# Kernel tuning notes

Measured on AMD Instinct MI355X. Metric: run time of the kernel, lower is better.

## Reference

```python
import jax, jax.numpy as jnp
import numpy as np

HIDDEN = 1024
HEADS = 16
HEAD_DIM = HIDDEN // HEADS
EPS = 1e-5


def setup_inputs() -> dict:
    key = jax.random.key(0)
    ks = jax.random.split(key, 9)
    B, S, H = 2, 2048, HIDDEN
    scale = 1.0 / np.sqrt(H)
    inp = {
        "hidden_states": jax.random.normal(ks[0], (B, S, H), dtype=jnp.float32),
        "Wq": jax.random.normal(ks[1], (H, H), dtype=jnp.float32) * scale,
        "bq": jnp.zeros((H,), jnp.float32),
        "Wk": jax.random.normal(ks[2], (H, H), dtype=jnp.float32) * scale,
        "bk": jnp.zeros((H,), jnp.float32),
        "Wv": jax.random.normal(ks[3], (H, H), dtype=jnp.float32) * scale,
        "bv": jnp.zeros((H,), jnp.float32),
        "Wo": jax.random.normal(ks[4], (H, H), dtype=jnp.float32) * scale,
        "bo": jnp.zeros((H,), jnp.float32),
        "gamma": jnp.ones((H,), jnp.float32),
        "beta": jnp.zeros((H,), jnp.float32),
    }
    return inp


def reference(hidden_states, Wq, bq, Wk, bk, Wv, bv, Wo, bo, gamma, beta):
    B, S, H = hidden_states.shape
    residual = hidden_states

    def shape(x):  # [B,S,H] -> [B,heads,S,head_dim]
        return x.reshape(B, S, HEADS, HEAD_DIM).transpose(0, 2, 1, 3)

    q = shape(hidden_states @ Wq + bq)
    k = shape(hidden_states @ Wk + bk)
    v = shape(hidden_states @ Wv + bv)

    scores = jnp.einsum("bhqd,bhkd->bhqk", q, k) / jnp.sqrt(
        jnp.asarray(HEAD_DIM, hidden_states.dtype))
    probs = jax.nn.softmax(scores, axis=-1)
    context = jnp.einsum("bhqk,bhkd->bhqd", probs, v)
    context = context.transpose(0, 2, 1, 3).reshape(B, S, H)

    output = context @ Wo + bo
    x = output + residual
    mu = jnp.mean(x, axis=-1, keepdims=True)
    var = jnp.mean(jnp.square(x - mu), axis=-1, keepdims=True)
    return (x - mu) * jax.lax.rsqrt(var + EPS) * gamma + beta
```

## Files before the change

### kernel.cpp

```cpp
#include <hip/hip_runtime.h>
#include <hip/hip_bf16.h>
#include <math.h>

#define HIDDEN 1024
#define HEADS 16
#define HEAD_DIM 64
#define EPS 1e-5f

typedef __attribute__((ext_vector_type(8))) short bf16x8;
typedef __attribute__((ext_vector_type(4))) float f32x4;

#if defined(__has_builtin)
#if __has_builtin(__builtin_amdgcn_exp2f)
#define EXP2(x) __builtin_amdgcn_exp2f(x)
#endif
#endif
#ifndef EXP2
#define EXP2(x) exp2f(x)
#endif

#define QSCALE 0.18033688011112042f

__device__ __forceinline__ short f2bf(float f) {
    union { float f; unsigned u; } v; v.f = f;
    unsigned r = v.u + 0x7fffu + ((v.u >> 16) & 1u);
    return (short)(r >> 16);
}

__global__ __launch_bounds__(256) void cast_bf16_kernel(
    const float* __restrict__ in, short* __restrict__ out, int n)
{
    int i = (blockIdx.x * 256 + threadIdx.x) * 4;
    if (i >= n) return;
    float4 v = *(const float4*)(in + i);
    short o[4] = { f2bf(v.x), f2bf(v.y), f2bf(v.z), f2bf(v.w) };
    *(uint2*)(out + i) = *(uint2*)o;
}

__global__ __launch_bounds__(256) void transpose_cast_kernel(
    const float* __restrict__ W, short* __restrict__ Wt, int Kd, int Nd,
    float scale)
{
    __shared__ short tile[32][33];
    int n0 = blockIdx.x * 32;
    int k0 = blockIdx.y * 32;
    int tx = threadIdx.x & 31;
    int ty = threadIdx.x >> 5;
    #pragma unroll
    for (int i = 0; i < 32; i += 8)
        tile[ty + i][tx] = f2bf(W[(size_t)(k0 + ty + i) * Nd + n0 + tx] * scale);
    __syncthreads();
    #pragma unroll
    for (int i = 0; i < 32; i += 8)
        Wt[(size_t)(n0 + ty + i) * Kd + k0 + tx] = tile[tx][ty + i];
}

__global__ __launch_bounds__(256) void concat_bias_kernel(
    const float* __restrict__ bq, const float* __restrict__ bk,
    const float* __restrict__ bv, float* __restrict__ b3)
{
    int i = blockIdx.x * 256 + threadIdx.x;
    if (i >= 3072) return;
    float v = (i < 1024) ? bq[i] * QSCALE
            : (i < 2048) ? bk[i - 1024] : bv[i - 2048];
    b3[i] = v;
}

__global__ __launch_bounds__(256) void gemm_bt_mfma(
    const short* __restrict__ A, const short* __restrict__ Bt,
    const float* __restrict__ bias,
    void* __restrict__ C0, int ldc0,
    void* __restrict__ C1, int split_col, int ldc1,
    int M, int N, int K, int out_bf16)
{
    __shared__ short As[128][40];
    __shared__ short Bs[128][40];
    const int tid = threadIdx.x;
    const int wave = tid >> 6, lane = tid & 63;
    const int ln16 = lane & 15, quad = lane >> 4;
    const int wm = (wave >> 1) * 64, wn = (wave & 1) * 64;
    const int brow = blockIdx.y * 128, bcol = blockIdx.x * 128;

    f32x4 acc[4][4];
    #pragma unroll
    for (int mt = 0; mt < 4; ++mt)
        #pragma unroll
        for (int nt = 0; nt < 4; ++nt) acc[mt][nt] = (f32x4){0.f, 0.f, 0.f, 0.f};

    for (int k0 = 0; k0 < K; k0 += 32) {
        #pragma unroll
        for (int i = 0; i < 2; ++i) {
            int idx = tid + i * 256;
            int r = idx >> 2;
            int c0 = (idx & 3) * 8;
            *(uint4*)&As[r][c0] = *(const uint4*)(A + (size_t)(brow + r) * K + k0 + c0);
            *(uint4*)&Bs[r][c0] = *(const uint4*)(Bt + (size_t)(bcol + r) * K + k0 + c0);
        }
        __syncthreads();
        bf16x8 af[4], bf[4];
        #pragma unroll
        for (int mt = 0; mt < 4; ++mt)
            af[mt] = *(const bf16x8*)&As[wm + mt * 16 + ln16][quad * 8];
        #pragma unroll
        for (int nt = 0; nt < 4; ++nt)
            bf[nt] = *(const bf16x8*)&Bs[wn + nt * 16 + ln16][quad * 8];
        #pragma unroll
        for (int mt = 0; mt < 4; ++mt)
            #pragma unroll
            for (int nt = 0; nt < 4; ++nt)
                acc[mt][nt] = __builtin_amdgcn_mfma_f32_16x16x32_bf16(
                    af[mt], bf[nt], acc[mt][nt], 0, 0, 0);
        __syncthreads();
    }

    void* Cp = C0; int ld = ldc0; int coff = 0;
    if (bcol >= split_col) { Cp = C1; ld = ldc1; coff = split_col; }

    #pragma unroll
    for (int mt = 0; mt < 4; ++mt) {
        #pragma unroll
        for (int r = 0; r < 4; ++r) {
            int row = brow + wm + mt * 16 + quad * 4 + r;
            #pragma unroll
            for (int nt = 0; nt < 4; ++nt) {
                int col = bcol + wn + nt * 16 + ln16;
                float v = acc[mt][nt][r] + bias[col];
                if (out_bf16) ((short*)Cp)[(size_t)row * ld + (col - coff)] = f2bf(v);
                else          ((float*)Cp)[(size_t)row * ld + (col - coff)] = v;
            }
        }
    }
}

__global__ __launch_bounds__(256) void vtranspose_kernel(
    const short* __restrict__ Vb, short* __restrict__ VT)
{
    __shared__ short t[64][72];
    const int c0 = blockIdx.x * 64;
    const int r0 = blockIdx.y * 64;
    const int tid = threadIdx.x;
    #pragma unroll
    for (int i = 0; i < 2; ++i) {
        int idx = tid + i * 256;
        int r = idx >> 3, cc = (idx & 7) * 8;
        *(uint4*)&t[r][cc] = *(const uint4*)(Vb + (size_t)(r0 + r) * 1024 + c0 + cc);
    }
    __syncthreads();
    #pragma unroll
    for (int i = 0; i < 2; ++i) {
        int idx = tid + i * 256;
        int c = idx >> 3, rr = (idx & 7) * 8;
        short tmp[8];
        #pragma unroll
        for (int j = 0; j < 8; ++j) tmp[j] = t[rr + j][c];
        *(uint4*)(VT + (size_t)(c0 + c) * 4096 + r0 + rr) = *(uint4*)tmp;
    }
}

__global__ __launch_bounds__(256) void attn_mfma_kernel(
    const short* __restrict__ QKb, const short* __restrict__ VT,
    short* __restrict__ Ctx)
{
    const int S = 2048;
    const int qt = blockIdx.x, h = blockIdx.y, b = blockIdx.z;
    const int tid = threadIdx.x;
    const int wave = tid >> 6, lane = tid & 63;
    const int ln16 = lane & 15, quad = lane >> 4;

    __shared__ short Ks[64][72];
    __shared__ short Vs[64][72];
    __shared__ short Ps[64][72];

    const size_t qrow = (size_t)(b * S + qt * 64 + wave * 16 + ln16);
    bf16x8 qfrag[2];
    qfrag[0] = *(const bf16x8*)(QKb + qrow * 2048 + h * 64 + quad * 8);
    qfrag[1] = *(const bf16x8*)(QKb + qrow * 2048 + h * 64 + 32 + quad * 8);

    bf16x8 ones;
    #pragma unroll
    for (int j = 0; j < 8; ++j) ones[j] = (short)0x3F80;

    f32x4 ofrag[4], lacc = (f32x4){0.f, 0.f, 0.f, 0.f};
    #pragma unroll
    for (int nt = 0; nt < 4; ++nt) ofrag[nt] = (f32x4){0.f, 0.f, 0.f, 0.f};

    for (int kt = 0; kt < S / 64; ++kt) {
        __syncthreads();
        #pragma unroll
        for (int i = 0; i < 2; ++i) {
            int idx = tid + i * 256;
            int r = idx >> 3, c0 = (idx & 7) * 8;
            *(uint4*)&Ks[r][c0] = *(const uint4*)(
                QKb + (size_t)(b * S + kt * 64 + r) * 2048 + 1024 + h * 64 + c0);
            *(uint4*)&Vs[r][c0] = *(const uint4*)(
                VT + (size_t)(h * 64 + r) * 4096 + b * S + kt * 64 + c0);
        }
        __syncthreads();

        f32x4 sf[4];
        #pragma unroll
        for (int nt = 0; nt < 4; ++nt) {
            f32x4 a = (f32x4){0.f, 0.f, 0.f, 0.f};
            a = __builtin_amdgcn_mfma_f32_16x16x32_bf16(
                *(const bf16x8*)&Ks[nt * 16 + ln16][quad * 8], qfrag[0], a, 0, 0, 0);
            a = __builtin_amdgcn_mfma_f32_16x16x32_bf16(
                *(const bf16x8*)&Ks[nt * 16 + ln16][32 + quad * 8], qfrag[1], a, 0, 0, 0);
            sf[nt] = a;
        }

        #pragma unroll
        for (int nt = 0; nt < 4; ++nt) {
            float p0 = EXP2(sf[nt][0]), p1 = EXP2(sf[nt][1]);
            float p2 = EXP2(sf[nt][2]), p3 = EXP2(sf[nt][3]);
            union { __hip_bfloat162 h2; unsigned u; } c01, c23;
            c01.h2 = __float22bfloat162_rn(make_float2(p0, p1));
            c23.h2 = __float22bfloat162_rn(make_float2(p2, p3));
            uint2 w; w.x = c01.u; w.y = c23.u;
            *(uint2*)&Ps[wave * 16 + ln16][nt * 16 + quad * 4] = w;
        }

        bf16x8 pf0 = *(const bf16x8*)&Ps[wave * 16 + ln16][quad * 8];
        bf16x8 pf1 = *(const bf16x8*)&Ps[wave * 16 + ln16][32 + quad * 8];
        lacc = __builtin_amdgcn_mfma_f32_16x16x32_bf16(pf0, ones, lacc, 0, 0, 0);
        lacc = __builtin_amdgcn_mfma_f32_16x16x32_bf16(pf1, ones, lacc, 0, 0, 0);
        #pragma unroll
        for (int nt = 0; nt < 4; ++nt) {
            f32x4 a = ofrag[nt];
            a = __builtin_amdgcn_mfma_f32_16x16x32_bf16(
                pf0, *(const bf16x8*)&Vs[nt * 16 + ln16][quad * 8], a, 0, 0, 0);
            a = __builtin_amdgcn_mfma_f32_16x16x32_bf16(
                pf1, *(const bf16x8*)&Vs[nt * 16 + ln16][32 + quad * 8], a, 0, 0, 0);
            ofrag[nt] = a;
        }
    }

    #pragma unroll
    for (int r = 0; r < 4; ++r) {
        float inv = 1.f / lacc[r];
        int row = b * S + qt * 64 + wave * 16 + quad * 4 + r;
        #pragma unroll
        for (int nt = 0; nt < 4; ++nt)
            Ctx[(size_t)row * 1024 + h * 64 + nt * 16 + ln16] =
                f2bf(ofrag[nt][r] * inv);
    }
}

__global__ __launch_bounds__(256) void resln_kernel(
    const float* __restrict__ proj, const float* __restrict__ resid,
    const float* __restrict__ gamma, const float* __restrict__ beta,
    float* __restrict__ out)
{
    const int rowi = blockIdx.x;
    const float* p = proj + (size_t)rowi * HIDDEN;
    const float* r = resid + (size_t)rowi * HIDDEN;
    float* o = out + (size_t)rowi * HIDDEN;
    const int tid = threadIdx.x;

    __shared__ float xs[HIDDEN];
    __shared__ float red[8];

    float local = 0.f;
    for (int i = tid; i < HIDDEN; i += 256) {
        float x = p[i] + r[i];
        xs[i] = x;
        local += x;
    }
    const int wid = tid >> 6, lane = tid & 63;
    #pragma unroll
    for (int off = 32; off > 0; off >>= 1) local += __shfl_down(local, off, 64);
    if (lane == 0) red[wid] = local;
    __syncthreads();
    float mu = (red[0] + red[1] + red[2] + red[3]) * (1.f / HIDDEN);

    float lv = 0.f;
    for (int i = tid; i < HIDDEN; i += 256) {
        float d = xs[i] - mu;
        lv += d * d;
    }
    #pragma unroll
    for (int off = 32; off > 0; off >>= 1) lv += __shfl_down(lv, off, 64);
    if (lane == 0) red[4 + wid] = lv;
    __syncthreads();
    float var = (red[4] + red[5] + red[6] + red[7]) * (1.f / HIDDEN);
    float rstd = rsqrtf(var + EPS);

    for (int i = tid; i < HIDDEN; i += 256) {
        o[i] = (xs[i] - mu) * rstd * gamma[i] + beta[i];
    }
}

extern "C" void kernel_launch(void* const* d_in, const int* in_sizes, int n_in,
                              void* d_out, int out_size, void* d_ws, size_t ws_size,
                              hipStream_t stream)
{
    const float* X     = (const float*)d_in[0];
    const float* Wq    = (const float*)d_in[1];
    const float* bq    = (const float*)d_in[2];
    const float* Wk    = (const float*)d_in[3];
    const float* bk    = (const float*)d_in[4];
    const float* Wv    = (const float*)d_in[5];
    const float* bv    = (const float*)d_in[6];
    const float* Wo    = (const float*)d_in[7];
    const float* bo    = (const float*)d_in[8];
    const float* gamma = (const float*)d_in[9];
    const float* beta  = (const float*)d_in[10];
    float* out = (float*)d_out;

    const int B = 2, S = 2048;
    const int M = B * S;
    const size_t mat = (size_t)M * HIDDEN;

    char* ws = (char*)d_ws;
    short* Xb  = (short*)(ws);
    short* VT  = (short*)(ws);
    short* Wot = (short*)(ws + (8ull << 20));
    short* Wt3 = (short*)(ws + (10ull << 20));
    float* b3  = (float*)(ws + (16ull << 20));
    short* QKb = (short*)(ws + (17ull << 20));
    float* Pj  = (float*)(ws + (17ull << 20));
    short* Vb  = (short*)(ws + (33ull << 20));
    short* Ctx = (short*)(ws + (33ull << 20));

    dim3 blk(256);

    cast_bf16_kernel<<<dim3((int)(mat / 4 + 255) / 256), blk, 0, stream>>>(X, Xb, (int)mat);

    dim3 tgrid(HIDDEN / 32, HIDDEN / 32);
    transpose_cast_kernel<<<tgrid, blk, 0, stream>>>(Wq, Wt3,                
                                                     HIDDEN, HIDDEN, QSCALE);
    transpose_cast_kernel<<<tgrid, blk, 0, stream>>>(Wk, Wt3 + 1024 * 1024,
                                                     HIDDEN, HIDDEN, 1.0f);
    transpose_cast_kernel<<<tgrid, blk, 0, stream>>>(Wv, Wt3 + 2048 * 1024,
                                                     HIDDEN, HIDDEN, 1.0f);
    transpose_cast_kernel<<<tgrid, blk, 0, stream>>>(Wo, Wot,
                                                     HIDDEN, HIDDEN, 1.0f);
    concat_bias_kernel<<<12, blk, 0, stream>>>(bq, bk, bv, b3);

    dim3 qkvgrid(3072 / 128, M / 128);
    gemm_bt_mfma<<<qkvgrid, blk, 0, stream>>>(Xb, Wt3, b3,
                                              QKb, 2048, Vb, 2048, 1024,
                                              M, 3072, HIDDEN, 1);

    vtranspose_kernel<<<dim3(16, 64), blk, 0, stream>>>(Vb, VT);

    dim3 agrid(S / 64, HEADS, B);
    attn_mfma_kernel<<<agrid, blk, 0, stream>>>(QKb, VT, Ctx);

    dim3 ogrid(HIDDEN / 128, M / 128);
    gemm_bt_mfma<<<ogrid, blk, 0, stream>>>(Ctx, Wot, bo,
                                            Pj, 1024, nullptr, 1 << 30, 0,
                                            M, HIDDEN, HIDDEN, 0);

    resln_kernel<<<M, blk, 0, stream>>>(Pj, X, gamma, beta, out);
}
```

Before: 266.8 us.

## Use direct global-to-LDS loads with swizzle, larger attention tiles, fused residual

The GEMM and attention kernels now load tiles with global_load_lds straight into LDS, using an XOR swizzle instead of padding to avoid bank conflicts. The attention kernel processes 128 query rows per block (two 16-row groups per wave), reusing each K/V tile across more queries, and its grid is reordered so heads vary fastest. The residual add moves into the output-projection GEMM epilogue and the layernorm becomes a vectorized float4 single pass. The four weight-transpose launches are merged into one. Risks are the more complex swizzle indexing and higher register use from the doubled attention accumulators.

```diff
diff --git a/kernel.cpp b/kernel.cpp
--- a/kernel.cpp
+++ b/kernel.cpp
@@ -27,6 +27,12 @@
     return (short)(r >> 16);
 }
 
+__device__ __forceinline__ void gl_lds16(const void* g, void* l) {
+    __builtin_amdgcn_global_load_lds(
+        (const __attribute__((address_space(1))) void*)g,
+        (__attribute__((address_space(3))) void*)l, 16, 0, 0);
+}
+
 __global__ __launch_bounds__(256) void cast_bf16_kernel(
     const float* __restrict__ in, short* __restrict__ out, int n)
 {
@@ -37,10 +43,16 @@
     *(uint2*)(out + i) = *(uint2*)o;
 }
 
-__global__ __launch_bounds__(256) void transpose_cast_kernel(
-    const float* __restrict__ W, short* __restrict__ Wt, int Kd, int Nd,
-    float scale)
-{
+__global__ __launch_bounds__(256) void wtrans_kernel(
+    const float* __restrict__ Wq, const float* __restrict__ Wk,
+    const float* __restrict__ Wv, const float* __restrict__ Wo,
+    short* __restrict__ Wt3, short* __restrict__ Wot)
+{
+    const int wsel = blockIdx.z;
+    const float* W = (wsel == 0) ? Wq : (wsel == 1) ? Wk : (wsel == 2) ? Wv : Wo;
+    short* dst = (wsel < 3) ? (Wt3 + (size_t)wsel * 1024 * 1024) : Wot;
+    const float scale = (wsel == 0) ? QSCALE : 1.0f;
+
     __shared__ short tile[32][33];
     int n0 = blockIdx.x * 32;
     int k0 = blockIdx.y * 32;
@@ -48,11 +60,11 @@
     int ty = threadIdx.x >> 5;
     #pragma unroll
     for (int i = 0; i < 32; i += 8)
-        tile[ty + i][tx] = f2bf(W[(size_t)(k0 + ty + i) * Nd + n0 + tx] * scale);
+        tile[ty + i][tx] = f2bf(W[(size_t)(k0 + ty + i) * 1024 + n0 + tx] * scale);
     __syncthreads();
     #pragma unroll
     for (int i = 0; i < 32; i += 8)
-        Wt[(size_t)(n0 + ty + i) * Kd + k0 + tx] = tile[tx][ty + i];
+        dst[(size_t)(n0 + ty + i) * 1024 + k0 + tx] = tile[tx][ty + i];
 }
 
 __global__ __launch_bounds__(256) void concat_bias_kernel(
@@ -71,16 +83,20 @@
     const float* __restrict__ bias,
     void* __restrict__ C0, int ldc0,
     void* __restrict__ C1, int split_col, int ldc1,
+    const float* __restrict__ resid,
     int M, int N, int K, int out_bf16)
 {
-    __shared__ short As[128][40];
-    __shared__ short Bs[128][40];
+    __shared__ short As[128 * 32];
+    __shared__ short Bs[128 * 32];
     const int tid = threadIdx.x;
     const int wave = tid >> 6, lane = tid & 63;
     const int ln16 = lane & 15, quad = lane >> 4;
     const int wm = (wave >> 1) * 64, wn = (wave & 1) * 64;
     const int brow = blockIdx.y * 128, bcol = blockIdx.x * 128;
 
+    const int sr  = lane >> 2;
+    const int scb = lane & 3;
+
     f32x4 acc[4][4];
     #pragma unroll
     for (int mt = 0; mt < 4; ++mt)
@@ -88,29 +104,34 @@
         for (int nt = 0; nt < 4; ++nt) acc[mt][nt] = (f32x4){0.f, 0.f, 0.f, 0.f};
 
     for (int k0 = 0; k0 < K; k0 += 32) {
+        __syncthreads();
         #pragma unroll
         for (int i = 0; i < 2; ++i) {
-            int idx = tid + i * 256;
-            int r = idx >> 2;
-            int c0 = (idx & 3) * 8;
-            *(uint4*)&As[r][c0] = *(const uint4*)(A + (size_t)(brow + r) * K + k0 + c0);
-            *(uint4*)&Bs[r][c0] = *(const uint4*)(Bt + (size_t)(bcol + r) * K + k0 + c0);
+            int rb = i * 64 + wave * 16;
+            int r  = rb + sr;
+            int csrc = (scb ^ ((r >> 1) & 3)) * 8;
+            gl_lds16(A  + (size_t)(brow + r) * K + k0 + csrc, &As[rb * 32]);
+            gl_lds16(Bt + (size_t)(bcol + r) * K + k0 + csrc, &Bs[rb * 32]);
         }
         __syncthreads();
+
         bf16x8 af[4], bf[4];
         #pragma unroll
-        for (int mt = 0; mt < 4; ++mt)
-            af[mt] = *(const bf16x8*)&As[wm + mt * 16 + ln16][quad * 8];
-        #pragma unroll
-        for (int nt = 0; nt < 4; ++nt)
-            bf[nt] = *(const bf16x8*)&Bs[wn + nt * 16 + ln16][quad * 8];
+        for (int mt = 0; mt < 4; ++mt) {
+            int r = wm + mt * 16 + ln16;
+            af[mt] = *(const bf16x8*)&As[r * 32 + ((quad ^ ((r >> 1) & 3)) * 8)];
+        }
+        #pragma unroll
+        for (int nt = 0; nt < 4; ++nt) {
+            int r = wn + nt * 16 + ln16;
+            bf[nt] = *(const bf16x8*)&Bs[r * 32 + ((quad ^ ((r >> 1) & 3)) * 8)];
+        }
         #pragma unroll
         for (int mt = 0; mt < 4; ++mt)
             #pragma unroll
             for (int nt = 0; nt < 4; ++nt)
                 acc[mt][nt] = __builtin_amdgcn_mfma_f32_16x16x32_bf16(
                     af[mt], bf[nt], acc[mt][nt], 0, 0, 0);
-        __syncthreads();
     }
 
     void* Cp = C0; int ld = ldc0; int coff = 0;
@@ -125,6 +146,7 @@
             for (int nt = 0; nt < 4; ++nt) {
                 int col = bcol + wn + nt * 16 + ln16;
                 float v = acc[mt][nt][r] + bias[col];
+                if (resid) v += resid[(size_t)row * N + col];
                 if (out_bf16) ((short*)Cp)[(size_t)row * ld + (col - coff)] = f2bf(v);
                 else          ((float*)Cp)[(size_t)row * ld + (col - coff)] = v;
             }
@@ -162,131 +184,156 @@
     short* __restrict__ Ctx)
 {
     const int S = 2048;
-    const int qt = blockIdx.x, h = blockIdx.y, b = blockIdx.z;
+    const int h = blockIdx.x, qt = blockIdx.y, b = blockIdx.z;
     const int tid = threadIdx.x;
     const int wave = tid >> 6, lane = tid & 63;
     const int ln16 = lane & 15, quad = lane >> 4;
 
-    __shared__ short Ks[64][72];
-    __shared__ short Vs[64][72];
-    __shared__ short Ps[64][72];
-
-    const size_t qrow = (size_t)(b * S + qt * 64 + wave * 16 + ln16);
-    bf16x8 qfrag[2];
-    qfrag[0] = *(const bf16x8*)(QKb + qrow * 2048 + h * 64 + quad * 8);
-    qfrag[1] = *(const bf16x8*)(QKb + qrow * 2048 + h * 64 + 32 + quad * 8);
+    __shared__ short Ks[64 * 64];
+    __shared__ short Vs[64 * 64];
+    __shared__ short Ps[128 * 72];
+
+    const int q0 = qt * 128 + wave * 32;
+
+    bf16x8 qfrag[2][2];
+    #pragma unroll
+    for (int qg = 0; qg < 2; ++qg)
+        #pragma unroll
+        for (int kb = 0; kb < 2; ++kb)
+            qfrag[qg][kb] = *(const bf16x8*)(QKb +
+                (size_t)(b * S + q0 + qg * 16 + ln16) * 2048 + h * 64 + kb * 32 + quad * 8);
 
     bf16x8 ones;
     #pragma unroll
     for (int j = 0; j < 8; ++j) ones[j] = (short)0x3F80;
 
-    f32x4 ofrag[4], lacc = (f32x4){0.f, 0.f, 0.f, 0.f};
-    #pragma unroll
-    for (int nt = 0; nt < 4; ++nt) ofrag[nt] = (f32x4){0.f, 0.f, 0.f, 0.f};
+    f32x4 of[2][4], lacc[2];
+    #pragma unroll
+    for (int qg = 0; qg < 2; ++qg) {
+        lacc[qg] = (f32x4){0.f, 0.f, 0.f, 0.f};
+        #pragma unroll
+        for (int nt = 0; nt < 4; ++nt) of[qg][nt] = (f32x4){0.f, 0.f, 0.f, 0.f};
+    }
+
+    const int sr  = lane >> 3;
+    const int scb = lane & 7;
 
     for (int kt = 0; kt < S / 64; ++kt) {
         __syncthreads();
         #pragma unroll
         for (int i = 0; i < 2; ++i) {
-            int idx = tid + i * 256;
-            int r = idx >> 3, c0 = (idx & 7) * 8;
-            *(uint4*)&Ks[r][c0] = *(const uint4*)(
-                QKb + (size_t)(b * S + kt * 64 + r) * 2048 + 1024 + h * 64 + c0);
-            *(uint4*)&Vs[r][c0] = *(const uint4*)(
-                VT + (size_t)(h * 64 + r) * 4096 + b * S + kt * 64 + c0);
+            int ci = wave * 2 + i;
+            int r  = ci * 8 + sr;
+            int csrc = ((scb ^ (r & 7))) * 8;
+            gl_lds16(QKb + (size_t)(b * S + kt * 64 + r) * 2048 + 1024 + h * 64 + csrc,
+                     &Ks[ci * 512]);
+            gl_lds16(VT + (size_t)(h * 64 + r) * 4096 + b * S + kt * 64 + csrc,
+                     &Vs[ci * 512]);
         }
         __syncthreads();
 
-        f32x4 sf[4];
         #pragma unroll
         for (int nt = 0; nt < 4; ++nt) {
-            f32x4 a = (f32x4){0.f, 0.f, 0.f, 0.f};
-            a = __builtin_amdgcn_mfma_f32_16x16x32_bf16(
-                *(const bf16x8*)&Ks[nt * 16 + ln16][quad * 8], qfrag[0], a, 0, 0, 0);
-            a = __builtin_amdgcn_mfma_f32_16x16x32_bf16(
-                *(const bf16x8*)&Ks[nt * 16 + ln16][32 + quad * 8], qfrag[1], a, 0, 0, 0);
-            sf[nt] = a;
-        }
-
+            bf16x8 kf[2];
+            #pragma unroll
+            for (int kb = 0; kb < 2; ++kb) {
+                int r = nt * 16 + ln16;
+                int cb = (kb * 4 + quad) ^ (r & 7);
+                kf[kb] = *(const bf16x8*)&Ks[r * 64 + cb * 8];
+            }
+            #pragma unroll
+            for (int qg = 0; qg < 2; ++qg) {
+                f32x4 a = (f32x4){0.f, 0.f, 0.f, 0.f};
+                a = __builtin_amdgcn_mfma_f32_16x16x32_bf16(kf[0], qfrag[qg][0], a, 0, 0, 0);
+                a = __builtin_amdgcn_mfma_f32_16x16x32_bf16(kf[1], qfrag[qg][1], a, 0, 0, 0);
+                float p0 = EXP2(a[0]), p1 = EXP2(a[1]);
+                float p2 = EXP2(a[2]), p3 = EXP2(a[3]);
+                union { __hip_bfloat162 h2; unsigned u; } c01, c23;
+                c01.h2 = __float22bfloat162_rn(make_float2(p0, p1));
+                c23.h2 = __float22bfloat162_rn(make_float2(p2, p3));
+                uint2 w; w.x = c01.u; w.y = c23.u;
+                *(uint2*)&Ps[(wave * 32 + qg * 16 + ln16) * 72 + nt * 16 + quad * 4] = w;
+            }
+        }
+
+        bf16x8 pf[2][2];
+        #pragma unroll
+        for (int qg = 0; qg < 2; ++qg)
+            #pragma unroll
+            for (int kb = 0; kb < 2; ++kb)
+                pf[qg][kb] = *(const bf16x8*)
+                    &Ps[(wave * 32 + qg * 16 + ln16) * 72 + kb * 32 + quad * 8];
+
+        #pragma unroll
+        for (int qg = 0; qg < 2; ++qg) {
+            lacc[qg] = __builtin_amdgcn_mfma_f32_16x16x32_bf16(pf[qg][0], ones, lacc[qg], 0, 0, 0);
+            lacc[qg] = __builtin_amdgcn_mfma_f32_16x16x32_bf16(pf[qg][1], ones, lacc[qg], 0, 0, 0);
+        }
         #pragma unroll
         for (int nt = 0; nt < 4; ++nt) {
-            float p0 = EXP2(sf[nt][0]), p1 = EXP2(sf[nt][1]);
-            float p2 = EXP2(sf[nt][2]), p3 = EXP2(sf[nt][3]);
-            union { __hip_bfloat162 h2; unsigned u; } c01, c23;
-            c01.h2 = __float22bfloat162_rn(make_float2(p0, p1));
-            c23.h2 = __float22bfloat162_rn(make_float2(p2, p3));
-            uint2 w; w.x = c01.u; w.y = c23.u;
-            *(uint2*)&Ps[wave * 16 + ln16][nt * 16 + quad * 4] = w;
-        }
-
-        bf16x8 pf0 = *(const bf16x8*)&Ps[wave * 16 + ln16][quad * 8];
-        bf16x8 pf1 = *(const bf16x8*)&Ps[wave * 16 + ln16][32 + quad * 8];
-        lacc = __builtin_amdgcn_mfma_f32_16x16x32_bf16(pf0, ones, lacc, 0, 0, 0);
-        lacc = __builtin_amdgcn_mfma_f32_16x16x32_bf16(pf1, ones, lacc, 0, 0, 0);
-        #pragma unroll
-        for (int nt = 0; nt < 4; ++nt) {
-            f32x4 a = ofrag[nt];
-            a = __builtin_amdgcn_mfma_f32_16x16x32_bf16(
-                pf0, *(const bf16x8*)&Vs[nt * 16 + ln16][quad * 8], a, 0, 0, 0);
-            a = __builtin_amdgcn_mfma_f32_16x16x32_bf16(
-                pf1, *(const bf16x8*)&Vs[nt * 16 + ln16][32 + quad * 8], a, 0, 0, 0);
-            ofrag[nt] = a;
-        }
-    }
-
-    #pragma unroll
-    for (int r = 0; r < 4; ++r) {
-        float inv = 1.f / lacc[r];
-        int row = b * S + qt * 64 + wave * 16 + quad * 4 + r;
-        #pragma unroll
-        for (int nt = 0; nt < 4; ++nt)
-            Ctx[(size_t)row * 1024 + h * 64 + nt * 16 + ln16] =
-                f2bf(ofrag[nt][r] * inv);
+            bf16x8 vf[2];
+            #pragma unroll
+            for (int kb = 0; kb < 2; ++kb) {
+                int r = nt * 16 + ln16;
+                int cb = (kb * 4 + quad) ^ (r & 7);
+                vf[kb] = *(const bf16x8*)&Vs[r * 64 + cb * 8];
+            }
+            #pragma unroll
+            for (int qg = 0; qg < 2; ++qg) {
+                of[qg][nt] = __builtin_amdgcn_mfma_f32_16x16x32_bf16(pf[qg][0], vf[0], of[qg][nt], 0, 0, 0);
+                of[qg][nt] = __builtin_amdgcn_mfma_f32_16x16x32_bf16(pf[qg][1], vf[1], of[qg][nt], 0, 0, 0);
+            }
+        }
+    }
+
+    #pragma unroll
+    for (int qg = 0; qg < 2; ++qg) {
+        #pragma unroll
+        for (int r = 0; r < 4; ++r) {
+            float inv = 1.f / lacc[qg][r];
+            int row = b * S + qt * 128 + wave * 32 + qg * 16 + quad * 4 + r;
+            #pragma unroll
+            for (int nt = 0; nt < 4; ++nt)
+                Ctx[(size_t)row * 1024 + h * 64 + nt * 16 + ln16] =
+                    f2bf(of[qg][nt][r] * inv);
+        }
     }
 }
 
 __global__ __launch_bounds__(256) void resln_kernel(
-    const float* __restrict__ proj, const float* __restrict__ resid,
-    const float* __restrict__ gamma, const float* __restrict__ beta,
-    float* __restrict__ out)
-{
-    const int rowi = blockIdx.x;
-    const float* p = proj + (size_t)rowi * HIDDEN;
-    const float* r = resid + (size_t)rowi * HIDDEN;
-    float* o = out + (size_t)rowi * HIDDEN;
+    const float* __restrict__ xin, const float* __restrict__ gamma,
+    const float* __restrict__ beta, float* __restrict__ out)
+{
+    const int row = blockIdx.x;
     const int tid = threadIdx.x;
-
-    __shared__ float xs[HIDDEN];
+    const int wid = tid >> 6, lane = tid & 63;
     __shared__ float red[8];
 
-    float local = 0.f;
-    for (int i = tid; i < HIDDEN; i += 256) {
-        float x = p[i] + r[i];
-        xs[i] = x;
-        local += x;
-    }
-    const int wid = tid >> 6, lane = tid & 63;
-    #pragma unroll
-    for (int off = 32; off > 0; off >>= 1) local += __shfl_down(local, off, 64);
-    if (lane == 0) red[wid] = local;
+    float4 x = *(const float4*)(xin + (size_t)row * HIDDEN + tid * 4);
+    float s = x.x + x.y + x.z + x.w;
+    #pragma unroll
+    for (int off = 32; off > 0; off >>= 1) s += __shfl_xor(s, off, 64);
+    if (lane == 0) red[wid] = s;
     __syncthreads();
     float mu = (red[0] + red[1] + red[2] + red[3]) * (1.f / HIDDEN);
 
-    float lv = 0.f;
-    for (int i = tid; i < HIDDEN; i += 256) {
-        float d = xs[i] - mu;
-        lv += d * d;
-    }
-    #pragma unroll
-    for (int off = 32; off > 0; off >>= 1) lv += __shfl_down(lv, off, 64);
-    if (lane == 0) red[4 + wid] = lv;
+    float dx = x.x - mu, dy = x.y - mu, dz = x.z - mu, dw = x.w - mu;
+    float v = dx * dx + dy * dy + dz * dz + dw * dw;
+    #pragma unroll
+    for (int off = 32; off > 0; off >>= 1) v += __shfl_xor(v, off, 64);
+    if (lane == 0) red[4 + wid] = v;
     __syncthreads();
     float var = (red[4] + red[5] + red[6] + red[7]) * (1.f / HIDDEN);
     float rstd = rsqrtf(var + EPS);
 
-    for (int i = tid; i < HIDDEN; i += 256) {
-        o[i] = (xs[i] - mu) * rstd * gamma[i] + beta[i];
-    }
+    float4 g = *(const float4*)(gamma + tid * 4);
+    float4 bt = *(const float4*)(beta + tid * 4);
+    float4 o;
+    o.x = dx * rstd * g.x + bt.x;
+    o.y = dy * rstd * g.y + bt.y;
+    o.z = dz * rstd * g.z + bt.z;
+    o.w = dw * rstd * g.w + bt.w;
+    *(float4*)(out + (size_t)row * HIDDEN + tid * 4) = o;
 }
 
 extern "C" void kernel_launch(void* const* d_in, const int* in_sizes, int n_in,
@@ -323,33 +370,24 @@
 
     dim3 blk(256);
 
-    cast_bf16_kernel<<<dim3((int)(mat / 4 + 255) / 256), blk, 0, stream>>>(X, Xb, (int)mat);
-
-    dim3 tgrid(HIDDEN / 32, HIDDEN / 32);
-    transpose_cast_kernel<<<tgrid, blk, 0, stream>>>(Wq, Wt3,                
-                                                     HIDDEN, HIDDEN, QSCALE);
-    transpose_cast_kernel<<<tgrid, blk, 0, stream>>>(Wk, Wt3 + 1024 * 1024,
-                                                     HIDDEN, HIDDEN, 1.0f);
-    transpose_cast_kernel<<<tgrid, blk, 0, stream>>>(Wv, Wt3 + 2048 * 1024,
-                                                     HIDDEN, HIDDEN, 1.0f);
-    transpose_cast_kernel<<<tgrid, blk, 0, stream>>>(Wo, Wot,
-                                                     HIDDEN, HIDDEN, 1.0f);
+    cast_bf16_kernel<<<dim3((int)(mat / 4 / 256)), blk, 0, stream>>>(X, Xb, (int)mat);
+    wtrans_kernel<<<dim3(32, 32, 4), blk, 0, stream>>>(Wq, Wk, Wv, Wo, Wt3, Wot);
     concat_bias_kernel<<<12, blk, 0, stream>>>(bq, bk, bv, b3);
 
     dim3 qkvgrid(3072 / 128, M / 128);
     gemm_bt_mfma<<<qkvgrid, blk, 0, stream>>>(Xb, Wt3, b3,
                                               QKb, 2048, Vb, 2048, 1024,
-                                              M, 3072, HIDDEN, 1);
+                                              nullptr, M, 3072, HIDDEN, 1);
 
     vtranspose_kernel<<<dim3(16, 64), blk, 0, stream>>>(Vb, VT);
 
-    dim3 agrid(S / 64, HEADS, B);
+    dim3 agrid(HEADS, S / 128, B);
     attn_mfma_kernel<<<agrid, blk, 0, stream>>>(QKb, VT, Ctx);
 
     dim3 ogrid(HIDDEN / 128, M / 128);
     gemm_bt_mfma<<<ogrid, blk, 0, stream>>>(Ctx, Wot, bo,
                                             Pj, 1024, nullptr, 1 << 30, 0,
-                                            M, HIDDEN, HIDDEN, 0);
-
-    resln_kernel<<<M, blk, 0, stream>>>(Pj, X, gamma, beta, out);
-}
+                                            X, M, HIDDEN, HIDDEN, 0);
+
+    resln_kernel<<<M, blk, 0, stream>>>(Pj, gamma, beta, out);
+}
```

New measurement: 243.6 us. 8.7% less time.
